# Performance work log

Measured on AMD Instinct MI355X. Metric: run time of the kernel, lower is better.

## Reference

```python
import jax, jax.numpy as jnp
import numpy as np

DIM, HEADS, DIM_HEAD = 1024, 16, 64
DIM_INNER = HEADS * DIM_HEAD  # 1024
SCALE = DIM_HEAD ** -0.5


def _rope(t):
    # t: [b, h, n, d]; interleaved-pair RoPE (lucidrains rotary-embedding-torch default)
    d = t.shape[-1]
    n = t.shape[-2]
    inv_freq = 1.0 / (10000.0 ** (jnp.arange(0, d, 2, dtype=jnp.float32) / d))
    angles = jnp.arange(n, dtype=jnp.float32)[:, None] * inv_freq[None, :]  # [n, d/2]
    cos, sin = jnp.cos(angles), jnp.sin(angles)
    t1, t2 = t[..., 0::2], t[..., 1::2]
    r1 = t1 * cos - t2 * sin
    r2 = t1 * sin + t2 * cos
    return jnp.stack([r1, r2], axis=-1).reshape(t.shape)


def setup_inputs() -> dict:
    key = jax.random.key(0)
    ks = jax.random.split(key, 8)
    b, n = 2, 2048
    inp = {
        "x": jax.random.normal(ks[0], (b, n, DIM), dtype=jnp.float32),
        "value_residual": jax.random.normal(ks[1], (b, HEADS, n, DIM_HEAD), dtype=jnp.float32),
        "gamma": jnp.ones((DIM,), dtype=jnp.float32),
        "w_qkv": jax.random.normal(ks[2], (DIM, 3 * DIM_INNER), dtype=jnp.float32) * (DIM ** -0.5),
        "w_mix": jax.random.normal(ks[3], (DIM, HEADS), dtype=jnp.float32) * (DIM ** -0.5),
        "b_mix": jnp.zeros((HEADS,), dtype=jnp.float32),
        "w_gates": jax.random.normal(ks[4], (DIM, HEADS), dtype=jnp.float32) * (DIM ** -0.5),
        "b_gates": jnp.zeros((HEADS,), dtype=jnp.float32),
        "w_out": jax.random.normal(ks[5], (DIM_INNER, DIM), dtype=jnp.float32) * (DIM_INNER ** -0.5),
    }
    return inp


def reference(x, value_residual, gamma, w_qkv, w_mix, b_mix, w_gates, b_gates, w_out):
    b, n, _ = x.shape
    # RMSNorm (lucidrains style: F.normalize * sqrt(dim) * gamma)
    norm = jnp.sqrt(jnp.sum(x * x, axis=-1, keepdims=True))
    xn = x / jnp.maximum(norm, 1e-12) * (DIM ** 0.5) * gamma

    qkv = xn @ w_qkv  # [b, n, 3*h*d]
    qkv = qkv.reshape(b, n, 3, HEADS, DIM_HEAD)
    q, k, v = [jnp.transpose(qkv[:, :, i], (0, 2, 1, 3)) for i in range(3)]  # [b,h,n,d]
    original_values = v

    # learned value-residual lerp
    mix = jax.nn.sigmoid(xn @ w_mix + b_mix)            # [b, n, h]
    mix = jnp.transpose(mix, (0, 2, 1))[..., None]       # [b, h, n, 1]
    v = v * (1.0 - mix) + value_residual * mix

    # rotary on q, k
    q = _rope(q)
    k = _rope(k)

    scores = jnp.einsum("bhid,bhjd->bhij", q, k) * SCALE
    attn = jax.nn.softmax(scores, axis=-1)
    out = jnp.einsum("bhij,bhjd->bhid", attn, v)         # [b, h, n, d]

    gates = jax.nn.sigmoid(xn @ w_gates + b_gates)       # [b, n, h]
    out = out * jnp.transpose(gates, (0, 2, 1))[..., None]

    out = jnp.transpose(out, (0, 2, 1, 3)).reshape(b, n, DIM_INNER)
    return out @ w_out, original_values
```

## Files before the change

kernel.cpp:

```cpp
#include <hip/hip_runtime.h>
#include <hip/hip_bf16.h>
#include <math.h>

#define DIMSZ 1024
#define HEADS 16
#define DHEAD 64
#define NSEQ  2048
#define BATCH 2
#define ROWS  (BATCH*NSEQ)
#define SCALE 0.125f
#define LOG2E 1.4426950408889634f

typedef __attribute__((ext_vector_type(8))) short short8;
typedef __attribute__((ext_vector_type(4))) float floatx4;
typedef __attribute__((ext_vector_type(16))) float floatx16;
typedef __attribute__((ext_vector_type(4))) unsigned uintx4;

#define MFMA16(a,b,c) __builtin_amdgcn_mfma_f32_16x16x32_bf16(a,b,c,0,0,0)
#define MFMA32(a,b,c) __builtin_amdgcn_mfma_f32_32x32x16_bf16(a,b,c,0,0,0)

__device__ __forceinline__ void gl2lds16(const void* g, void* l) {
    __builtin_amdgcn_global_load_lds(
        (const __attribute__((address_space(1))) unsigned int*)g,
        (__attribute__((address_space(3))) unsigned int*)l, 16, 0, 0);
}

__device__ __forceinline__ unsigned short bf16r(float a) {
    unsigned u = __float_as_uint(a);
    u += 0x7fff + ((u >> 16) & 1);
    return (unsigned short)(u >> 16);
}
__device__ __forceinline__ unsigned pack_bf16(float a, float b) {
    unsigned ua = __float_as_uint(a), ub = __float_as_uint(b);
    ua += 0x7fff + ((ua >> 16) & 1);
    ub += 0x7fff + ((ub >> 16) & 1);
    return (ua >> 16) | (ub & 0xffff0000u);
}
__device__ __forceinline__ float2 bf2f(unsigned u) {
    float2 r;
    r.x = __uint_as_float(u << 16);
    r.y = __uint_as_float(u & 0xffff0000u);
    return r;
}
__device__ __forceinline__ unsigned cvtpk(float lo, float hi) {
    unsigned r;
    asm("v_cvt_pk_bf16_f32 %0, %1, %2" : "=v"(r) : "v"(lo), "v"(hi));
    return r;
}
__device__ __forceinline__ void pl32swap(unsigned &a, unsigned &b) {
#if __has_builtin(__builtin_amdgcn_permlane32_swap)
    auto r = __builtin_amdgcn_permlane32_swap(a, b, false, false);
    a = (unsigned)r[0]; b = (unsigned)r[1];
#else
    asm volatile("v_permlane32_swap_b32 %0, %1" : "+v"(a), "+v"(b));
#endif
}
__device__ __forceinline__ float fexp2(float x) {
#if __has_builtin(__builtin_amdgcn_exp2f)
    return __builtin_amdgcn_exp2f(x);
#else
    return exp2f(x);
#endif
}
__device__ __forceinline__ float fsin_rev(float x) {
#if __has_builtin(__builtin_amdgcn_sinf)
    return __builtin_amdgcn_sinf(x);
#else
    return __sinf(x * 6.28318530717958647692f);
#endif
}
__device__ __forceinline__ float fcos_rev(float x) {
#if __has_builtin(__builtin_amdgcn_cosf)
    return __builtin_amdgcn_cosf(x);
#else
    return __cosf(x * 6.28318530717958647692f);
#endif
}

#define SWZ(row) (((row) & 7) ^ (((row) >> 3) & 1))

__global__ __launch_bounds__(256) void prep_kernel(
    const float* __restrict__ x, const float* __restrict__ gamma,
    const float* __restrict__ w_qkv, const float* __restrict__ w_out,
    const float* __restrict__ w_mix, const float* __restrict__ w_gates,
    unsigned short* __restrict__ xnb,
    unsigned short* __restrict__ wqkvT, unsigned short* __restrict__ woutT,
    unsigned short* __restrict__ wmgT, float* __restrict__ rtab)
{
    __shared__ float t[32][33];
    __shared__ float wred[4];
    const int bid = blockIdx.x;
    const int tid = threadIdx.x;

    if (bid < ROWS) {
        const int row = bid;
        const float4 xv = ((const float4*)(x + (size_t)row * DIMSZ))[tid];
        float ss = xv.x*xv.x + xv.y*xv.y + xv.z*xv.z + xv.w*xv.w;
        #pragma unroll
        for (int off = 1; off < 64; off <<= 1) ss += __shfl_xor(ss, off);
        if ((tid & 63) == 0) wred[tid >> 6] = ss;
        __syncthreads();
        const float total = wred[0] + wred[1] + wred[2] + wred[3];
        const float inv = 32.0f / fmaxf(sqrtf(total), 1e-12f);
        const float4 gv = ((const float4*)gamma)[tid];
        uint2 pk;
        pk.x = pack_bf16(xv.x * inv * gv.x, xv.y * inv * gv.y);
        pk.y = pack_bf16(xv.z * inv * gv.z, xv.w * inv * gv.w);
        ((uint2*)(xnb + (size_t)row * DIMSZ))[tid] = pk;
        return;
    }

    const int tb = bid - ROWS;
    const int bx = tb % 130;
    const int k0 = (tb / 130) * 32;
    const int tx = tid & 31, tyy = tid >> 5;
    if (bx < 128) {
        const float* src;
        unsigned short* dst;
        int N, n0;
        if (bx < 96) { src = w_qkv; dst = wqkvT; N = 3*DIMSZ; n0 = bx*32; }
        else         { src = w_out; dst = woutT; N = DIMSZ;   n0 = (bx-96)*32; }
        #pragma unroll
        for (int i = 0; i < 4; i++)
            t[tyy*4 + i][tx] = src[(size_t)(k0 + tyy*4 + i)*N + n0 + tx];
        __syncthreads();
        #pragma unroll
        for (int i = 0; i < 4; i++)
            dst[(size_t)(n0 + tyy*4 + i)*DIMSZ + k0 + tx] = bf16r(t[tx][tyy*4 + i]);
    } else if (bx == 128) {
        #pragma unroll
        for (int i = 0; i < 4; i++) {
            const int kk = k0 + tyy*4 + i;
            t[tyy*4 + i][tx] = (tx < 16) ? w_mix[kk*16 + tx]
                                         : w_gates[kk*16 + (tx - 16)];
        }
        __syncthreads();
        #pragma unroll
        for (int i = 0; i < 4; i++)
            wmgT[(size_t)(tyy*4 + i)*DIMSZ + k0 + tx] = bf16r(t[tx][tyy*4 + i]);
    } else {
        const int pos = (k0 >> 5)*64 + (tid >> 2);
        const int f0 = (tid & 3) * 8;
        float2* dst = (float2*)rtab + (size_t)pos*32 + f0;
        #pragma unroll
        for (int tt = 0; tt < 8; tt++) {
            const float pf = (float)(f0 + tt);
            const float rev = (float)pos * fexp2(-pf * 0.41524101186092029f
                                                 - 2.6514961294723187f);
            const float rf = rev - floorf(rev);
            float2 cs;
            cs.x = fcos_rev(rf);
            cs.y = fsin_rev(rf);
            dst[tt] = cs;
        }
    }
}

__global__ __launch_bounds__(256) void mix_gates_mfma(
    const unsigned short* __restrict__ A, const unsigned short* __restrict__ WG,
    const float* __restrict__ b_mix, const float* __restrict__ b_gates,
    float* __restrict__ mixo, float* __restrict__ gateso)
{
    __shared__ short As[4][2][32*32];
    __shared__ short Bs[4][2][32*32];
    __shared__ float red[4][32*32];
    const int tid = threadIdx.x;
    const int wv = tid >> 6, lane = tid & 63;
    const int g = lane >> 4, c = lane & 15;
    const int bm = blockIdx.x * 32;
    const int kbase = wv * 256;

    floatx4 acc[2][2];
    #pragma unroll
    for (int mt = 0; mt < 2; mt++)
        #pragma unroll
        for (int nt = 0; nt < 2; nt++) acc[mt][nt] = (floatx4){0.f,0.f,0.f,0.f};

    #pragma unroll
    for (int r = 0; r < 2; r++) {
        const int ch = lane + 64*r;
        const int row = ch >> 2, cc = ch & 3;
        gl2lds16(A  + (size_t)(bm + row)*DIMSZ + kbase + cc*8, (void*)(&As[wv][0][0] + ch*8));
        gl2lds16(WG + (size_t)row*DIMSZ        + kbase + cc*8, (void*)(&Bs[wv][0][0] + ch*8));
    }
    for (int i = 0; i < 8; i++) {
        const int cur = i & 1;
        if (i < 7) {
            const int k0 = kbase + (i + 1)*32;
            #pragma unroll
            for (int r = 0; r < 2; r++) {
                const int ch = lane + 64*r;
                const int row = ch >> 2, cc = ch & 3;
                gl2lds16(A  + (size_t)(bm + row)*DIMSZ + k0 + cc*8, (void*)(&As[wv][cur^1][0] + ch*8));
                gl2lds16(WG + (size_t)row*DIMSZ        + k0 + cc*8, (void*)(&Bs[wv][cur^1][0] + ch*8));
            }
            asm volatile("s_waitcnt vmcnt(4)" ::: "memory");
        } else {
            asm volatile("s_waitcnt vmcnt(0)" ::: "memory");
        }
        __builtin_amdgcn_sched_barrier(0);
        short8 af[2], bf[2];
        #pragma unroll
        for (int mt = 0; mt < 2; mt++) af[mt] = *(const short8*)(&As[wv][cur][0] + (mt*16 + c)*32 + g*8);
        #pragma unroll
        for (int nt = 0; nt < 2; nt++) bf[nt] = *(const short8*)(&Bs[wv][cur][0] + (nt*16 + c)*32 + g*8);
        #pragma unroll
        for (int mt = 0; mt < 2; mt++)
            #pragma unroll
            for (int nt = 0; nt < 2; nt++)
                acc[mt][nt] = MFMA16(af[mt], bf[nt], acc[mt][nt]);
    }
    #pragma unroll
    for (int mt = 0; mt < 2; mt++)
        #pragma unroll
        for (int nt = 0; nt < 2; nt++)
            #pragma unroll
            for (int r2 = 0; r2 < 4; r2++)
                red[wv][(mt*16 + g*4 + r2)*32 + nt*16 + c] = acc[mt][nt][r2];
    __syncthreads();
    #pragma unroll
    for (int jj = 0; jj < 4; jj++) {
        const int idx = tid + jj*256;
        const int row = idx >> 5, col = idx & 31;
        const float s = (red[0][idx] + red[1][idx]) + (red[2][idx] + red[3][idx]);
        if (col < 16) {
            const float lm = s + b_mix[col];
            mixo[(size_t)(bm + row)*HEADS + col] = 1.0f / (1.0f + fexp2(-lm * LOG2E));
        } else {
            const float lg = s + b_gates[col - 16];
            gateso[(size_t)(bm + row)*HEADS + (col - 16)] = 1.0f / (1.0f + fexp2(-lg * LOG2E));
        }
    }
}

__device__ __forceinline__ void stage_qkv(
    const unsigned short* A, const unsigned short* BT,
    short* as, short* bs, int bm, int bn, int kk, int tid)
{
    #pragma unroll
    for (int r = 0; r < 2; r++) {
        const int ch = tid + 256*r;
        const int row = ch >> 2, j = ch & 3;
        gl2lds16(A  + (size_t)(bm + row)*DIMSZ + kk + j*8, (void*)(as + ch*8));
        gl2lds16(BT + (size_t)(bn + row)*DIMSZ + kk + j*8, (void*)(bs + ch*8));
    }
}

__global__ __launch_bounds__(256) void gemm_qkv_mfma(
    const unsigned short* __restrict__ A, const unsigned short* __restrict__ BT,
    unsigned short* __restrict__ qb, unsigned short* __restrict__ kb,
    float* __restrict__ vb)
{
    __shared__ short As[3][128*32];
    __shared__ short Bs[3][128*32];
    const int tid = threadIdx.x;
    const int wv = tid >> 6, lane = tid & 63;
    const int g = lane >> 4, c = lane & 15;
    const int wm = wv >> 1, wn = wv & 1;

    const int id = blockIdx.y * gridDim.x + blockIdx.x;
    const int xcd = id & 7, j = id >> 3;
    const int bnb = (xcd & 1)*12 + (j % 12);
    const int byb = (xcd >> 1)*8 + (j / 12);
    const int bm = byb * 128, bn = bnb * 128;

    floatx4 acc[4][4];
    #pragma unroll
    for (int mt = 0; mt < 4; mt++)
        #pragma unroll
        for (int nt = 0; nt < 4; nt++) acc[mt][nt] = (floatx4){0.f,0.f,0.f,0.f};

    stage_qkv(A, BT, &As[0][0], &Bs[0][0], bm, bn, 0,  tid);
    stage_qkv(A, BT, &As[1][0], &Bs[1][0], bm, bn, 32, tid);
    asm volatile("s_waitcnt vmcnt(4)" ::: "memory");
    __builtin_amdgcn_s_barrier();
    __builtin_amdgcn_sched_barrier(0);

    int cur = 0, nxt = 2;
    for (int i = 0; i < 32; i++) {
        const int k0 = i*32;
        if (i < 30)
            stage_qkv(A, BT, &As[nxt][0], &Bs[nxt][0], bm, bn, k0 + 64, tid);

        short8 af[4], bf[4];
        #pragma unroll
        for (int mt = 0; mt < 4; mt++) af[mt] = *(const short8*)(&As[cur][0] + (wm*64 + mt*16 + c)*32 + g*8);
        #pragma unroll
        for (int nt = 0; nt < 4; nt++) bf[nt] = *(const short8*)(&Bs[cur][0] + (wn*64 + nt*16 + c)*32 + g*8);
        __builtin_amdgcn_s_setprio(1);
        #pragma unroll
        for (int mt = 0; mt < 4; mt++)
            #pragma unroll
            for (int nt = 0; nt < 4; nt++)
                acc[mt][nt] = MFMA16(af[mt], bf[nt], acc[mt][nt]);
        __builtin_amdgcn_s_setprio(0);

        if (i < 31) {
            if (i < 30) asm volatile("s_waitcnt vmcnt(4)" ::: "memory");
            else        asm volatile("s_waitcnt vmcnt(0)" ::: "memory");
            __builtin_amdgcn_s_barrier();
            __builtin_amdgcn_sched_barrier(0);
        }
        cur = (cur == 2) ? 0 : cur + 1;
        nxt = (nxt == 2) ? 0 : nxt + 1;
    }
    __syncthreads();

    const int i3 = bn >> 10;
    const int nb = bn - (i3 << 10);
    if (i3 < 2) {
        unsigned short* dst = (i3 == 0) ? qb : kb;
        float* wbuf = (float*)(&As[0][0]) + wv*1088;
        const int rd_row = lane >> 2, seg = lane & 3;
        #pragma unroll
        for (int mt = 0; mt < 4; mt++) {
            #pragma unroll
            for (int nt = 0; nt < 4; nt++)
                #pragma unroll
                for (int r2 = 0; r2 < 4; r2++)
                    wbuf[(g*4 + r2)*68 + nt*16 + c] = acc[mt][nt][r2];
            __builtin_amdgcn_s_waitcnt(0xc07f);
            const float* rp = wbuf + rd_row*68 + seg*16;
            const float4 f0 = *(const float4*)(rp + 0);
            const float4 f1 = *(const float4*)(rp + 4);
            const float4 f2 = *(const float4*)(rp + 8);
            const float4 f3 = *(const float4*)(rp + 12);
            unsigned o[8];
            o[0] = cvtpk(f0.x, f0.y); o[1] = cvtpk(f0.z, f0.w);
            o[2] = cvtpk(f1.x, f1.y); o[3] = cvtpk(f1.z, f1.w);
            o[4] = cvtpk(f2.x, f2.y); o[5] = cvtpk(f2.z, f2.w);
            o[6] = cvtpk(f3.x, f3.y); o[7] = cvtpk(f3.z, f3.w);
            const int row = bm + wm*64 + mt*16 + rd_row;
            const int col = nb + wn*64 + seg*16;
            const int hh = col >> 6, dd = col & 63;
            const int bb2 = row >> 11, pos = row & 2047;
            unsigned short* dp = dst + (((size_t)(bb2*HEADS + hh)*NSEQ) + pos)*DHEAD + dd;
            *(uint4*)dp = (uint4){o[0], o[1], o[2], o[3]};
            *(uint4*)(dp + 8) = (uint4){o[4], o[5], o[6], o[7]};
            __builtin_amdgcn_s_waitcnt(0xc07f);
        }
    } else {
        #pragma unroll
        for (int mt = 0; mt < 4; mt++)
            #pragma unroll
            for (int nt = 0; nt < 4; nt++)
                #pragma unroll
                for (int r2 = 0; r2 < 4; r2++) {
                    const int row = bm + wm*64 + mt*16 + g*4 + r2;
                    const int col = nb + wn*64 + nt*16 + c;
                    const int hh = col >> 6, dd = col & 63;
                    const int bb2 = row >> 11, pos = row & 2047;
                    vb[(((size_t)(bb2*HEADS + hh)*NSEQ) + pos)*DHEAD + dd] = acc[mt][nt][r2];
                }
    }
}

__global__ __launch_bounds__(256) void rope_blend_kernel2(
    unsigned short* __restrict__ q, unsigned short* __restrict__ k,
    const float* __restrict__ vorig, const float* __restrict__ vres,
    const float* __restrict__ mixb, const float* __restrict__ rtab,
    unsigned short* __restrict__ vT)
{
    __shared__ unsigned short vt[64*72];
    const int tid = threadIdx.x;
    const int bh = blockIdx.y, bb = bh >> 4, h = bh & 15;
    const int p0 = blockIdx.x * 64;
    {
        const int pr = tid >> 2, d0 = (tid & 3) * 16;
        const int pos = p0 + pr;
        const size_t base = ((size_t)bh*NSEQ + pos)*DHEAD + d0;

        float cs_sn[16];
        #pragma unroll
        for (int i = 0; i < 4; i++)
            *(float4*)(cs_sn + i*4) = *(const float4*)(rtab + (size_t)pos*64 + d0 + i*4);

        uint4 qr0 = *(uint4*)(q + base), qr1 = *(uint4*)(q + base + 8);
        uint4 kr0 = *(uint4*)(k + base), kr1 = *(uint4*)(k + base + 8);
        unsigned qw[8] = {qr0.x, qr0.y, qr0.z, qr0.w, qr1.x, qr1.y, qr1.z, qr1.w};
        unsigned kw[8] = {kr0.x, kr0.y, kr0.z, kr0.w, kr1.x, kr1.y, kr1.z, kr1.w};
        const float QSC = SCALE * LOG2E;
        #pragma unroll
        for (int j = 0; j < 8; j++) {
            const float cs = cs_sn[2*j], sn = cs_sn[2*j + 1];
            float2 qv = bf2f(qw[j]);
            float2 kv = bf2f(kw[j]);
            const float q1 = qv.x*cs - qv.y*sn, q2 = qv.x*sn + qv.y*cs;
            const float k1 = kv.x*cs - kv.y*sn, k2 = kv.x*sn + kv.y*cs;
            qw[j] = pack_bf16(q1*QSC, q2*QSC);
            kw[j] = pack_bf16(k1, k2);
        }
        *(uint4*)(q + base)     = *(uint4*)(qw + 0);
        *(uint4*)(q + base + 8) = *(uint4*)(qw + 4);
        *(uint4*)(k + base)     = *(uint4*)(kw + 0);
        *(uint4*)(k + base + 8) = *(uint4*)(kw + 4);

        float vv[16], vr[16];
        #pragma unroll
        for (int i = 0; i < 4; i++) {
            *(float4*)(vv + i*4) = *(const float4*)(vorig + base + i*4);
            *(float4*)(vr + i*4) = *(const float4*)(vres + base + i*4);
        }
        const float mx = mixb[((size_t)(bb*NSEQ + pos))*HEADS + h];
        #pragma unroll
        for (int j = 0; j < 8; j++) {
            const float b0 = vv[2*j]*(1.f-mx)   + vr[2*j]*mx;
            const float b1 = vv[2*j+1]*(1.f-mx) + vr[2*j+1]*mx;
            vt[pr*72 + d0 + 2*j]     = bf16r(b0);
            vt[pr*72 + d0 + 2*j + 1] = bf16r(b1);
        }
    }
    __syncthreads();
    {
        const int dd = tid >> 2, c0 = (tid & 3) * 16;
        unsigned o[8];
        #pragma unroll
        for (int j = 0; j < 8; j++) {
            const unsigned a  = vt[(c0 + 2*j)*72 + dd];
            const unsigned b2 = vt[(c0 + 2*j + 1)*72 + dd];
            o[j] = a | (b2 << 16);
        }
        unsigned short* dst = vT + ((size_t)bh*DHEAD + dd)*NSEQ + p0 + c0;
        *(uint4*)(dst)     = *(uint4*)(o + 0);
        *(uint4*)(dst + 8) = *(uint4*)(o + 4);
    }
}

__global__ __launch_bounds__(256, 4) void attn_mfma_kernel(
    const unsigned short* __restrict__ qg,
    const unsigned short* __restrict__ kg,
    const unsigned short* __restrict__ vT,
    unsigned short* __restrict__ Op0,
    unsigned short* __restrict__ Op1,
    float* __restrict__ lpart)
{
    __shared__ short Kt[2][64*64];
    __shared__ short Vt[2][64*64];

    const int tid = threadIdx.x;
    const int w = tid >> 6, lane = tid & 63;
    const int hi = lane >> 5, cq = lane & 31;

    int wg = blockIdx.y * gridDim.x + blockIdx.x;
    wg = (wg & 7) * 128 + (wg >> 3);
    const int q0 = (wg & 15) * 128;
    const int byy = wg >> 4;
    const int bh = byy >> 1, s = byy & 1;
    const int bb = bh >> 4, h = bh & 15;

    short8 qf[4];
    #pragma unroll
    for (int kd = 0; kd < 4; kd++)
        qf[kd] = *(const short8*)(qg + ((size_t)bh*NSEQ + q0 + w*32 + cq)*DHEAD + kd*16 + hi*8);

    floatx16 O0{}, O1{};
    float lsum = 0.f;

    const unsigned short* kbase = kg + (size_t)bh*NSEQ*DHEAD;
    const unsigned short* vbase = vT + (size_t)bh*DHEAD*NSEQ;

    {
        const int kt = s*16;
        #pragma unroll
        for (int r = 0; r < 2; r++) {
            const int ch = tid + 256*r;
            const int row = ch >> 3;
            const int u = (ch & 7) ^ SWZ(row);
            gl2lds16(kbase + (size_t)(kt*64 + row)*DHEAD + u*8, (void*)(&Kt[0][0] + ch*8));
            gl2lds16(vbase + (size_t)row*NSEQ + kt*64 + u*8,   (void*)(&Vt[0][0] + ch*8));
        }
    }
    __syncthreads();

    for (int i = 0; i < 16; i++) {
        const int cur = i & 1;
        const short* Ktc = &Kt[cur][0];
        const short* Vtc = &Vt[cur][0];

        if (i < 15) {
            const int kt = s*16 + i + 1;
            short* Ktn = &Kt[cur ^ 1][0];
            short* Vtn = &Vt[cur ^ 1][0];
            #pragma unroll
            for (int r = 0; r < 2; r++) {
                const int ch = tid + 256*r;
                const int row = ch >> 3;
                const int u = (ch & 7) ^ SWZ(row);
                gl2lds16(kbase + (size_t)(kt*64 + row)*DHEAD + u*8, (void*)(Ktn + ch*8));
                gl2lds16(vbase + (size_t)row*NSEQ + kt*64 + u*8,   (void*)(Vtn + ch*8));
            }
        }

        floatx16 accS0{}, accS1{};
        __builtin_amdgcn_s_setprio(1);
        #pragma unroll
        for (int kd = 0; kd < 4; kd++) {
            const int r0 = cq, r1 = 32 + cq;
            short8 kf0 = *(const short8*)(Ktc + r0*64 + (((kd*2 + hi) ^ SWZ(r0)) * 8));
            short8 kf1 = *(const short8*)(Ktc + r1*64 + (((kd*2 + hi) ^ SWZ(r1)) * 8));
            accS0 = MFMA32(kf0, qf[kd], accS0);
            accS1 = MFMA32(kf1, qf[kd], accS1);
        }
        __builtin_amdgcn_s_setprio(0);

        #pragma unroll
        for (int kt2 = 0; kt2 < 2; kt2++) {
            const floatx16 accS = kt2 ? accS1 : accS0;

            float p[16];
            #pragma unroll
            for (int r = 0; r < 16; r++) p[r] = fexp2(accS[r]);
            const float a1 = (p[0]+p[1]) + (p[2]+p[3]);
            const float a2 = (p[4]+p[5]) + (p[6]+p[7]);
            const float a3 = (p[8]+p[9]) + (p[10]+p[11]);
            const float a4 = (p[12]+p[13]) + (p[14]+p[15]);
            lsum += (a1+a2) + (a3+a4);

            unsigned d0 = cvtpk(p[0],  p[1]);
            unsigned d1 = cvtpk(p[2],  p[3]);
            unsigned d2 = cvtpk(p[4],  p[5]);
            unsigned d3 = cvtpk(p[6],  p[7]);
            unsigned d4 = cvtpk(p[8],  p[9]);
            unsigned d5 = cvtpk(p[10], p[11]);
            unsigned d6 = cvtpk(p[12], p[13]);
            unsigned d7 = cvtpk(p[14], p[15]);
            pl32swap(d0, d2);
            pl32swap(d1, d3);
            pl32swap(d4, d6);
            pl32swap(d5, d7);
            const uintx4 t0 = {d0, d1, d2, d3};
            const uintx4 t1 = {d4, d5, d6, d7};
            const short8 pf0 = __builtin_bit_cast(short8, t0);
            const short8 pf1 = __builtin_bit_cast(short8, t1);

            __builtin_amdgcn_s_setprio(1);
            #pragma unroll
            for (int ks2 = 0; ks2 < 2; ks2++) {
                const short8 pf = ks2 ? pf1 : pf0;
                #pragma unroll
                for (int nt2 = 0; nt2 < 2; nt2++) {
                    const int rv = nt2*32 + cq;
                    short8 vf = *(const short8*)(Vtc + rv*64 + (((kt2*4 + ks2*2 + hi) ^ SWZ(rv)) * 8));
                    if (nt2 == 0) O0 = MFMA32(pf, vf, O0);
                    else          O1 = MFMA32(pf, vf, O1);
                }
            }
            __builtin_amdgcn_s_setprio(0);
        }
        __syncthreads();
    }

    unsigned short* Op = s ? Op1 : Op0;
    float l = lsum + __shfl_xor(lsum, 32);
    if (hi == 0)
        lpart[((size_t)s*ROWS + bb*NSEQ + q0 + w*32 + cq)*HEADS + h] = l;
    #pragma unroll
    for (int reg = 0; reg < 16; reg++) {
        const int qq = (reg & 3) + 8*(reg >> 2) + 4*hi;
        const int rowg = q0 + w*32 + qq;
        unsigned short* op = Op + ((size_t)(bb*NSEQ + rowg))*DIMSZ + h*DHEAD + cq;
        op[0]  = bf16r(O0[reg]);
        op[32] = bf16r(O1[reg]);
    }
}

__global__ __launch_bounds__(256) void attn_combine_kernel(
    const unsigned short* __restrict__ Op1, const float* __restrict__ lpart,
    const float* __restrict__ gates, unsigned short* __restrict__ attnO)
{
    const int idx = blockIdx.x * 256 + threadIdx.x;
    const int row = idx >> 7;
    const int c8 = (idx & 127) * 8;
    const int h = c8 >> 6;
    const float l0 = lpart[(size_t)row*HEADS + h];
    const float l1 = lpart[((size_t)ROWS + row)*HEADS + h];
    const float gt = gates[(size_t)row*HEADS + h];
    const float sc = gt / (l0 + l1);
    const size_t base = (size_t)row*DIMSZ + c8;
    const uint4 a = *(const uint4*)(attnO + base);
    const uint4 b = *(const uint4*)(Op1 + base);
    const unsigned aw[4] = {a.x, a.y, a.z, a.w};
    const unsigned bw[4] = {b.x, b.y, b.z, b.w};
    unsigned o[4];
    #pragma unroll
    for (int j = 0; j < 4; j++) {
        const float2 fa = bf2f(aw[j]);
        const float2 fb = bf2f(bw[j]);
        o[j] = pack_bf16((fa.x + fb.x)*sc, (fa.y + fb.y)*sc);
    }
    *(uint4*)(attnO + base) = *(uint4*)o;
}

__device__ __forceinline__ void stage_out(
    const unsigned short* A, const unsigned short* BT,
    short* as, short* bs, int bm, int bn, int kk, int tid)
{
    const int row = tid >> 2, j = tid & 3;
    gl2lds16(A  + (size_t)(bm + row)*DIMSZ + kk + j*8, (void*)(as + tid*8));
    gl2lds16(BT + (size_t)(bn + row)*DIMSZ + kk + j*8, (void*)(bs + tid*8));
}

__global__ __launch_bounds__(256) void gemm_out_mfma(
    const unsigned short* __restrict__ A, const unsigned short* __restrict__ BT,
    float* __restrict__ out0)
{
    __shared__ short As[3][64*32];
    __shared__ short Bs[3][64*32];
    const int tid = threadIdx.x;
    const int wv = tid >> 6, lane = tid & 63;
    const int g = lane >> 4, c = lane & 15;
    const int wm = wv >> 1, wn = wv & 1;

    const int id = blockIdx.y * gridDim.x + blockIdx.x;
    const int xcd = id & 7, j = id >> 3;
    const int bnb = j & 15, byb = xcd*8 + (j >> 4);
    const int bm = byb * 64, bn = bnb * 64;

    floatx4 acc[2][2];
    #pragma unroll
    for (int mt = 0; mt < 2; mt++)
        #pragma unroll
        for (int nt = 0; nt < 2; nt++) acc[mt][nt] = (floatx4){0.f,0.f,0.f,0.f};

    stage_out(A, BT, &As[0][0], &Bs[0][0], bm, bn, 0,  tid);
    stage_out(A, BT, &As[1][0], &Bs[1][0], bm, bn, 32, tid);
    asm volatile("s_waitcnt vmcnt(2)" ::: "memory");
    __builtin_amdgcn_s_barrier();
    __builtin_amdgcn_sched_barrier(0);

    int cur = 0, nxt = 2;
    for (int i = 0; i < 32; i++) {
        const int k0 = i*32;
        if (i < 30)
            stage_out(A, BT, &As[nxt][0], &Bs[nxt][0], bm, bn, k0 + 64, tid);

        short8 af[2], bf[2];
        #pragma unroll
        for (int mt = 0; mt < 2; mt++) af[mt] = *(const short8*)(&As[cur][0] + (wm*32 + mt*16 + c)*32 + g*8);
        #pragma unroll
        for (int nt = 0; nt < 2; nt++) bf[nt] = *(const short8*)(&Bs[cur][0] + (wn*32 + nt*16 + c)*32 + g*8);
        __builtin_amdgcn_s_setprio(1);
        #pragma unroll
        for (int mt = 0; mt < 2; mt++)
            #pragma unroll
            for (int nt = 0; nt < 2; nt++)
                acc[mt][nt] = MFMA16(af[mt], bf[nt], acc[mt][nt]);
        __builtin_amdgcn_s_setprio(0);

        if (i < 31) {
            if (i < 30) asm volatile("s_waitcnt vmcnt(2)" ::: "memory");
            else        asm volatile("s_waitcnt vmcnt(0)" ::: "memory");
            __builtin_amdgcn_s_barrier();
            __builtin_amdgcn_sched_barrier(0);
        }
        cur = (cur == 2) ? 0 : cur + 1;
        nxt = (nxt == 2) ? 0 : nxt + 1;
    }

    #pragma unroll
    for (int mt = 0; mt < 2; mt++)
        #pragma unroll
        for (int nt = 0; nt < 2; nt++)
            #pragma unroll
            for (int r2 = 0; r2 < 4; r2++) {
                const int row = bm + wm*32 + mt*16 + g*4 + r2;
                const int col = bn + wn*32 + nt*16 + c;
                out0[(size_t)row*DIMSZ + col] = acc[mt][nt][r2];
            }
}

extern "C" void kernel_launch(void* const* d_in, const int* in_sizes, int n_in,
                              void* d_out, int out_size, void* d_ws, size_t ws_size,
                              hipStream_t stream) {
    const float* x       = (const float*)d_in[0];
    const float* vres    = (const float*)d_in[1];
    const float* gamma   = (const float*)d_in[2];
    const float* w_qkv   = (const float*)d_in[3];
    const float* w_mix   = (const float*)d_in[4];
    const float* b_mix   = (const float*)d_in[5];
    const float* w_gates = (const float*)d_in[6];
    const float* b_gates = (const float*)d_in[7];
    const float* w_out   = (const float*)d_in[8];

    float* out0 = (float*)d_out;
    float* out1 = out0 + (size_t)ROWS * DIMSZ;

    char* ws = (char*)d_ws;
    unsigned short* xnb   = (unsigned short*)(ws);
    unsigned short* wqkvT = (unsigned short*)(ws + (8u<<20));
    unsigned short* woutT = (unsigned short*)(ws + (14u<<20));
    unsigned short* qb2   = (unsigned short*)(ws + (16u<<20));
    unsigned short* kb2   = (unsigned short*)(ws + (24u<<20));
    unsigned short* vT    = (unsigned short*)(ws + (32u<<20));
    unsigned short* attnO = (unsigned short*)(ws + (40u<<20));
    float*          mixb  = (float*)(ws + (48u<<20));
    float*          gatesb= (float*)(ws + (48u<<20) + 262144);
    unsigned short* wmgT  = (unsigned short*)(ws + (49u<<20));
    unsigned short* Op1   = (unsigned short*)(ws + (50u<<20));
    float*          lpart = (float*)(ws + (58u<<20));
    float*          rtab  = (float*)(ws + (59u<<20));

    prep_kernel<<<ROWS + 130*(DIMSZ/32), 256, 0, stream>>>(
        x, gamma, w_qkv, w_out, w_mix, w_gates, xnb, wqkvT, woutT, wmgT, rtab);

    mix_gates_mfma<<<ROWS/32, 256, 0, stream>>>(
        xnb, wmgT, b_mix, b_gates, mixb, gatesb);

    gemm_qkv_mfma<<<dim3(3*DIMSZ/128, ROWS/128), 256, 0, stream>>>(
        xnb, wqkvT, qb2, kb2, out1);

    rope_blend_kernel2<<<dim3(NSEQ/64, BATCH*HEADS), 256, 0, stream>>>(
        qb2, kb2, out1, vres, mixb, rtab, vT);

    attn_mfma_kernel<<<dim3(NSEQ/128, BATCH*HEADS*2), 256, 0, stream>>>(
        qb2, kb2, vT, attnO, Op1, lpart);

    attn_combine_kernel<<<ROWS*DIMSZ/8/256, 256, 0, stream>>>(
        Op1, lpart, gatesb, attnO);

    gemm_out_mfma<<<dim3(DIMSZ/64, ROWS/64), 256, 0, stream>>>(
        attnO, woutT, out0);
}
```

Baseline: 227.5 us.

## Fuse split-KV attention combine and gating into the output projection GEMM

Removes the separate combine kernel. The output GEMM now loads both partial attention outputs through registers, scales them by gate/(l0+l1) from a per-block LDS table, and writes the combined bf16 tile into LDS before running the MFMAs. This drops one launch and a full read/write pass over the attention buffer. In exchange, the partials are re-read by every column block (16x redundant A traffic, though mostly L2-served), the buffering drops from triple to double, and register-path loads replace direct global-to-LDS loads with a full __syncthreads each iteration.

```diff
diff --git a/kernel.cpp b/kernel.cpp
--- a/kernel.cpp
+++ b/kernel.cpp
@@ -564,48 +564,14 @@
     }
 }
 
-__global__ __launch_bounds__(256) void attn_combine_kernel(
-    const unsigned short* __restrict__ Op1, const float* __restrict__ lpart,
-    const float* __restrict__ gates, unsigned short* __restrict__ attnO)
+__global__ __launch_bounds__(256) void gemm_out_fused(
+    const unsigned short* __restrict__ Op0, const unsigned short* __restrict__ Op1,
+    const float* __restrict__ lpart, const float* __restrict__ gates,
+    const unsigned short* __restrict__ BT, float* __restrict__ out0)
 {
-    const int idx = blockIdx.x * 256 + threadIdx.x;
-    const int row = idx >> 7;
-    const int c8 = (idx & 127) * 8;
-    const int h = c8 >> 6;
-    const float l0 = lpart[(size_t)row*HEADS + h];
-    const float l1 = lpart[((size_t)ROWS + row)*HEADS + h];
-    const float gt = gates[(size_t)row*HEADS + h];
-    const float sc = gt / (l0 + l1);
-    const size_t base = (size_t)row*DIMSZ + c8;
-    const uint4 a = *(const uint4*)(attnO + base);
-    const uint4 b = *(const uint4*)(Op1 + base);
-    const unsigned aw[4] = {a.x, a.y, a.z, a.w};
-    const unsigned bw[4] = {b.x, b.y, b.z, b.w};
-    unsigned o[4];
-    #pragma unroll
-    for (int j = 0; j < 4; j++) {
-        const float2 fa = bf2f(aw[j]);
-        const float2 fb = bf2f(bw[j]);
-        o[j] = pack_bf16((fa.x + fb.x)*sc, (fa.y + fb.y)*sc);
-    }
-    *(uint4*)(attnO + base) = *(uint4*)o;
-}
-
-__device__ __forceinline__ void stage_out(
-    const unsigned short* A, const unsigned short* BT,
-    short* as, short* bs, int bm, int bn, int kk, int tid)
-{
-    const int row = tid >> 2, j = tid & 3;
-    gl2lds16(A  + (size_t)(bm + row)*DIMSZ + kk + j*8, (void*)(as + tid*8));
-    gl2lds16(BT + (size_t)(bn + row)*DIMSZ + kk + j*8, (void*)(bs + tid*8));
-}
-
-__global__ __launch_bounds__(256) void gemm_out_mfma(
-    const unsigned short* __restrict__ A, const unsigned short* __restrict__ BT,
-    float* __restrict__ out0)
-{
-    __shared__ short As[3][64*32];
-    __shared__ short Bs[3][64*32];
+    __shared__ short As[2][64*32];
+    __shared__ short Bs[2][64*32];
+    __shared__ float scs[64*16];
     const int tid = threadIdx.x;
     const int wv = tid >> 6, lane = tid & 63;
     const int g = lane >> 4, c = lane & 15;
@@ -616,23 +582,51 @@
     const int bnb = j & 15, byb = xcd*8 + (j >> 4);
     const int bm = byb * 64, bn = bnb * 64;
 
+    const int arow = tid >> 2, aseg = tid & 3;
+
+    uint4 a0 = *(const uint4*)(Op0 + (size_t)(bm + arow)*DIMSZ + aseg*8);
+    uint4 a1 = *(const uint4*)(Op1 + (size_t)(bm + arow)*DIMSZ + aseg*8);
+    gl2lds16(BT + (size_t)(bn + arow)*DIMSZ + aseg*8, (void*)(&Bs[0][0] + tid*8));
+
+    #pragma unroll
+    for (int e = 0; e < 4; e++) {
+        const int n = tid + e*256;
+        const int r = n >> 4, h = n & 15;
+        const int row = bm + r;
+        const float l0 = lpart[(size_t)row*HEADS + h];
+        const float l1 = lpart[((size_t)ROWS + row)*HEADS + h];
+        scs[n] = gates[(size_t)row*HEADS + h] / (l0 + l1);
+    }
+    __syncthreads();
+    {
+        const float sc = scs[arow*16 + 0];
+        const unsigned aw[4] = {a0.x, a0.y, a0.z, a0.w};
+        const unsigned bw[4] = {a1.x, a1.y, a1.z, a1.w};
+        unsigned o[4];
+        #pragma unroll
+        for (int jj = 0; jj < 4; jj++) {
+            const float2 fa = bf2f(aw[jj]);
+            const float2 fb = bf2f(bw[jj]);
+            o[jj] = cvtpk((fa.x + fb.x)*sc, (fa.y + fb.y)*sc);
+        }
+        *(uint4*)(&As[0][0] + arow*32 + aseg*8) = (uint4){o[0], o[1], o[2], o[3]};
+    }
+    __syncthreads();
+
     floatx4 acc[2][2];
     #pragma unroll
     for (int mt = 0; mt < 2; mt++)
         #pragma unroll
         for (int nt = 0; nt < 2; nt++) acc[mt][nt] = (floatx4){0.f,0.f,0.f,0.f};
 
-    stage_out(A, BT, &As[0][0], &Bs[0][0], bm, bn, 0,  tid);
-    stage_out(A, BT, &As[1][0], &Bs[1][0], bm, bn, 32, tid);
-    asm volatile("s_waitcnt vmcnt(2)" ::: "memory");
-    __builtin_amdgcn_s_barrier();
-    __builtin_amdgcn_sched_barrier(0);
-
-    int cur = 0, nxt = 2;
     for (int i = 0; i < 32; i++) {
-        const int k0 = i*32;
-        if (i < 30)
-            stage_out(A, BT, &As[nxt][0], &Bs[nxt][0], bm, bn, k0 + 64, tid);
+        const int cur = i & 1;
+        if (i < 31) {
+            const int k0 = (i + 1)*32;
+            a0 = *(const uint4*)(Op0 + (size_t)(bm + arow)*DIMSZ + k0 + aseg*8);
+            a1 = *(const uint4*)(Op1 + (size_t)(bm + arow)*DIMSZ + k0 + aseg*8);
+            gl2lds16(BT + (size_t)(bn + arow)*DIMSZ + k0 + aseg*8, (void*)(&Bs[cur^1][0] + tid*8));
+        }
 
         short8 af[2], bf[2];
         #pragma unroll
@@ -648,13 +642,19 @@
         __builtin_amdgcn_s_setprio(0);
 
         if (i < 31) {
-            if (i < 30) asm volatile("s_waitcnt vmcnt(2)" ::: "memory");
-            else        asm volatile("s_waitcnt vmcnt(0)" ::: "memory");
-            __builtin_amdgcn_s_barrier();
-            __builtin_amdgcn_sched_barrier(0);
-        }
-        cur = (cur == 2) ? 0 : cur + 1;
-        nxt = (nxt == 2) ? 0 : nxt + 1;
+            const float sc = scs[arow*16 + ((i + 1) >> 1)];
+            const unsigned aw[4] = {a0.x, a0.y, a0.z, a0.w};
+            const unsigned bw[4] = {a1.x, a1.y, a1.z, a1.w};
+            unsigned o[4];
+            #pragma unroll
+            for (int jj = 0; jj < 4; jj++) {
+                const float2 fa = bf2f(aw[jj]);
+                const float2 fb = bf2f(bw[jj]);
+                o[jj] = cvtpk((fa.x + fb.x)*sc, (fa.y + fb.y)*sc);
+            }
+            *(uint4*)(&As[cur^1][0] + arow*32 + aseg*8) = (uint4){o[0], o[1], o[2], o[3]};
+        }
+        __syncthreads();
     }
 
     #pragma unroll
@@ -692,7 +692,7 @@
     unsigned short* qb2   = (unsigned short*)(ws + (16u<<20));
     unsigned short* kb2   = (unsigned short*)(ws + (24u<<20));
     unsigned short* vT    = (unsigned short*)(ws + (32u<<20));
-    unsigned short* attnO = (unsigned short*)(ws + (40u<<20));
+    unsigned short* Op0   = (unsigned short*)(ws + (40u<<20));
     float*          mixb  = (float*)(ws + (48u<<20));
     float*          gatesb= (float*)(ws + (48u<<20) + 262144);
     unsigned short* wmgT  = (unsigned short*)(ws + (49u<<20));
@@ -713,11 +713,8 @@
         qb2, kb2, out1, vres, mixb, rtab, vT);
 
     attn_mfma_kernel<<<dim3(NSEQ/128, BATCH*HEADS*2), 256, 0, stream>>>(
-        qb2, kb2, vT, attnO, Op1, lpart);
-
-    attn_combine_kernel<<<ROWS*DIMSZ/8/256, 256, 0, stream>>>(
-        Op1, lpart, gatesb, attnO);
-
-    gemm_out_mfma<<<dim3(DIMSZ/64, ROWS/64), 256, 0, stream>>>(
-        attnO, woutT, out0);
-}
+        qb2, kb2, vT, Op0, Op1, lpart);
+
+    gemm_out_fused<<<dim3(DIMSZ/64, ROWS/64), 256, 0, stream>>>(
+        Op0, Op1, lpart, gatesb, woutT, out0);
+}
```

After: 226.0 us. Within noise of the previous version (-0.7%).
